# Performance work log

Hardware: AMD Instinct MI355X
Metric: run time of the kernel (lower is better)

Reference implementation:

```python
import jax, jax.numpy as jnp
import numpy as np


def _unfold(x, kh, kw):
    # torch.nn.functional.unfold ordering: channel-major, then kernel row, then kernel col
    B, C, H, W = x.shape
    Ho, Wo = H - kh + 1, W - kw + 1
    cols = jnp.stack([x[:, :, i:i + Ho, j:j + Wo]
                      for i in range(kh) for j in range(kw)], axis=2)  # [B,C,kh*kw,Ho,Wo]
    return cols.reshape(B, C * kh * kw, Ho * Wo), Ho, Wo


def _conv_unfold_matmul(x, w, b):
    # preprocessing: unfold -> A [B,L,K], B = w.view(O,-1).T [K,O]
    # matmul -> [B,L,O]; postprocessing: transpose, reshape, add bias
    O = w.shape[0]
    kh, kw = w.shape[2], w.shape[3]
    cols, Ho, Wo = _unfold(x, kh, kw)                      # [B,K,L]
    out = jnp.einsum('bkl,ok->bol', cols, w.reshape(O, -1))  # [B,O,L]
    return out.reshape(x.shape[0], O, Ho, Wo) + b[None, :, None, None]


def setup_inputs() -> dict:
    key = jax.random.key(0)
    ks = jax.random.split(key, 9)
    B = 4096
    x = jax.random.normal(ks[0], (B, 1, 28, 28), dtype=jnp.float32)
    w1 = jax.random.normal(ks[1], (10, 1, 10, 10), dtype=jnp.float32) * 0.1
    b1 = jax.random.normal(ks[2], (10,), dtype=jnp.float32) * 0.1
    w2 = jax.random.normal(ks[3], (20, 10, 10, 10), dtype=jnp.float32) * 0.03
    b2 = jax.random.normal(ks[4], (20,), dtype=jnp.float32) * 0.1
    w3 = jax.random.normal(ks[5], (20, 20, 5, 5), dtype=jnp.float32) * 0.04
    b3 = jax.random.normal(ks[6], (20,), dtype=jnp.float32) * 0.1
    wf = jax.random.normal(ks[7], (10, 720), dtype=jnp.float32) * 0.04
    bf = jax.random.normal(ks[8], (10,), dtype=jnp.float32) * 0.1
    return {"x": x, "w1": w1, "b1": b1, "w2": w2, "b2": b2,
            "w3": w3, "b3": b3, "wf": wf, "bf": bf}


def reference(x, w1, b1, w2, b2, w3, b3, wf, bf):
    h = jax.nn.relu(_conv_unfold_matmul(x, w1, b1))   # [B,10,19,19]
    h = jax.nn.relu(_conv_unfold_matmul(h, w2, b2))   # [B,20,10,10]
    h = jax.nn.relu(_conv_unfold_matmul(h, w3, b3))   # [B,20,6,6]
    h = h.reshape(-1, 720)
    return h @ wf.T + bf                               # [B,10]
```

## Files before the change

kernel.cpp:

```cpp
#include <hip/hip_runtime.h>


typedef short s16x4 __attribute__((ext_vector_type(4)));
typedef short s16x8 __attribute__((ext_vector_type(8)));
typedef float f32x4 __attribute__((ext_vector_type(4)));

#define ROW1 248
#define ROW2 248
#define XOFF 4712
#define SM_BYTES 11024

static __device__ __forceinline__ unsigned short f2bf(float f) {
    union { float f; unsigned int u; } v; v.f = f;
    unsigned int u = v.u;
    unsigned int r = (u + 0x7fffu + ((u >> 16) & 1u)) >> 16;
    return (unsigned short)r;
}

static __device__ __forceinline__ s16x8 cat8(s16x4 lo, s16x4 hi) {
    return __builtin_shufflevector(lo, hi, 0, 1, 2, 3, 4, 5, 6, 7);
}

__global__ __launch_bounds__(256) void wprep_k(const float* __restrict__ w1,
                                               const float* __restrict__ w2,
                                               const float* __restrict__ w3,
                                               unsigned short* __restrict__ wbuf) {
    int e = blockIdx.x * 256 + threadIdx.x;
    if (e < 40960) {
        int t = e & 7, lane = (e >> 3) & 63, nt = (e >> 9) & 1;
        int ck = (e >> 10) & 3, i = e >> 12;
        int k = ck * 32 + ((lane >> 4) & 3) * 8 + t;
        int o = nt * 16 + (lane & 15);
        int j = k / 12, c = k % 12;
        float val = (j < 10 && c < 10 && o < 20) ? w2[o * 1000 + c * 100 + i * 10 + j] : 0.f;
        wbuf[e] = f2bf(val);
    } else if (e < 61440) {
        int e2 = e - 40960;
        int t = e2 & 7, lane = (e2 >> 3) & 63, nt = (e2 >> 9) & 1;
        int ck = (e2 >> 10) & 3, i = e2 >> 12;
        int k = ck * 32 + ((lane >> 4) & 3) * 8 + t;
        int o = nt * 16 + (lane & 15);
        int j = k / 20, c = k % 20;
        float val = (j < 5 && o < 20) ? w3[o * 500 + c * 25 + i * 5 + j] : 0.f;
        wbuf[e] = f2bf(val);
    } else {
        int e2 = e - 61440;
        int t = e2 & 7, lane = (e2 >> 3) & 63;
        int kc = (e2 >> 9) % 9, nt = (e2 >> 9) / 9;
        int n = nt * 16 + (lane & 15);
        int k = kc * 32 + ((lane >> 4) & 3) * 8 + t;
        float val = 0.f;
        if (n < 190 && k < 280) {
            int ox = n / 10, o = n - ox * 10;
            int i = k / 28, xc = k - i * 28;
            int j = xc - ox;
            if (j >= 0 && j < 10) val = w1[o * 100 + i * 10 + j];
        }
        wbuf[61440 + e2] = f2bf(val);
    }
}

__global__ __launch_bounds__(128, 4) void fused_k(const float* __restrict__ x,
                                                  const float* __restrict__ b1,
                                                  const unsigned short* __restrict__ wbuf2,
                                                  const unsigned short* __restrict__ wbuf3,
                                                  const unsigned short* __restrict__ wband,
                                                  const float* __restrict__ b2,
                                                  const float* __restrict__ b3,
                                                  const float* __restrict__ wf,
                                                  const float* __restrict__ bf,
                                                  float* __restrict__ out) {
    __shared__ __align__(16) unsigned char smem[SM_BYTES];
    unsigned short* sm16 = (unsigned short*)smem;
    unsigned short* h1  = sm16;
    unsigned short* xbf = sm16 + XOFF;
    unsigned short* h2s = sm16;
    float*          h3s = (float*)smem;
    float*          fcp = (float*)(smem + 2880);

    const int tid = threadIdx.x;
    const int wave = tid >> 6, lane = tid & 63;
    const int b = blockIdx.x;
    const int quad = lane >> 4, lm = lane & 15;

    {
        const float4* src = (const float4*)(x + (size_t)b * 784);
        for (int k = tid; k < 196; k += 128) {
            float4 v = src[k];
            s16x4 p = { (short)f2bf(v.x), (short)f2bf(v.y),
                        (short)f2bf(v.z), (short)f2bf(v.w) };
            *(s16x4*)(xbf + k * 4) = p;
        }
        if (tid < 16) xbf[784 + tid] = 0;
        for (int e = tid; e < 95; e += 128) {
            int row = e / 5, seg = e - row * 5;
            *(s16x4*)(h1 + row * ROW1 + 228 + seg * 4) = (s16x4){0, 0, 0, 0};
        }
        for (int e = tid; e < 361; e += 128) {
            int oy = e / 19, ox = e - oy * 19;
            *(unsigned int*)(h1 + oy * ROW1 + ox * 12 + 10) = 0u;
        }
    }
    __syncthreads();

    {
        int m1 = lm + 16; if (m1 > 18) m1 = 18;
        const unsigned short* ab0 = xbf + lm * 28 + quad * 8;
        const unsigned short* ab1 = xbf + m1 * 28 + quad * 8;
        const unsigned short* wb = wband + lane * 8;
        f32x4 acc1[6][2] = {};
#pragma unroll
        for (int kc = 0; kc < 9; ++kc) {
            s16x8 a0 = cat8(*(const s16x4*)(ab0 + kc * 32),
                            *(const s16x4*)(ab0 + kc * 32 + 4));
            s16x8 a1 = cat8(*(const s16x4*)(ab1 + kc * 32),
                            *(const s16x4*)(ab1 + kc * 32 + 4));
#pragma unroll
            for (int q = 0; q < 6; ++q) {
                int nt = wave * 6 + q;
                s16x8 bw = *(const s16x8*)(wb + (nt * 9 + kc) * 512);
                acc1[q][0] = __builtin_amdgcn_mfma_f32_16x16x32_bf16(a0, bw, acc1[q][0], 0, 0, 0);
                acc1[q][1] = __builtin_amdgcn_mfma_f32_16x16x32_bf16(a1, bw, acc1[q][1], 0, 0, 0);
            }
        }
#pragma unroll
        for (int q = 0; q < 6; ++q) {
            int n = (wave * 6 + q) * 16 + lm;
            if (n < 190) {
                int ox = n / 10, o = n - ox * 10;
                float bias = b1[o];
#pragma unroll
                for (int mt = 0; mt < 2; ++mt) {
#pragma unroll
                    for (int r = 0; r < 4; ++r) {
                        int oy = mt * 16 + quad * 4 + r;
                        if (oy < 19)
                            h1[oy * ROW1 + ox * 12 + o] =
                                f2bf(fmaxf(acc1[q][mt][r] + bias, 0.f));
                    }
                }
            }
        }
    }
    __syncthreads();

    int abase[4];
#pragma unroll
    for (int mt = 0; mt < 4; ++mt) {
        int tg = (wave == 0) ? mt : 4 + mt;
        int m = tg * 16 + lm;
        if (m > 99) m = 99;
        int y = m / 10, xx = m - 10 * y;
        abase[mt] = y * ROW1 + xx * 12 + quad * 8;
    }
    f32x4 acc[4][2] = {};
    {
        const unsigned short* wptr = wbuf2 + lane * 8;
        s16x8 wc0 = *(const s16x8*)(wptr);
        s16x8 wc1 = *(const s16x8*)(wptr + 512);
        s16x8 afc[4], afn[4];
        {
            const unsigned short* sbi = h1;
#pragma unroll
            for (int mt = 0; mt < 3; ++mt)
                afc[mt] = cat8(*(const s16x4*)(sbi + abase[mt]),
                               *(const s16x4*)(sbi + abase[mt] + 4));
            if (wave == 0)
                afc[3] = cat8(*(const s16x4*)(sbi + abase[3]),
                              *(const s16x4*)(sbi + abase[3] + 4));
            else
                afc[3] = afc[2];
        }
#pragma unroll
        for (int it = 0; it < 40; ++it) {
            s16x8 wn0 = *(const s16x8*)(wptr + (it + 1) * 1024);
            s16x8 wn1 = *(const s16x8*)(wptr + (it + 1) * 1024 + 512);
            const unsigned short* sbn = h1 + ((it + 1) >> 2) * ROW1 + ((it + 1) & 3) * 32;
#pragma unroll
            for (int mt = 0; mt < 3; ++mt)
                afn[mt] = cat8(*(const s16x4*)(sbn + abase[mt]),
                               *(const s16x4*)(sbn + abase[mt] + 4));
            if (wave == 0)
                afn[3] = cat8(*(const s16x4*)(sbn + abase[3]),
                              *(const s16x4*)(sbn + abase[3] + 4));
            else
                afn[3] = afc[3];
#pragma unroll
            for (int mt = 0; mt < 3; ++mt) {
                acc[mt][0] = __builtin_amdgcn_mfma_f32_16x16x32_bf16(afc[mt], wc0, acc[mt][0], 0, 0, 0);
                acc[mt][1] = __builtin_amdgcn_mfma_f32_16x16x32_bf16(afc[mt], wc1, acc[mt][1], 0, 0, 0);
            }
            if (wave == 0) {
                acc[3][0] = __builtin_amdgcn_mfma_f32_16x16x32_bf16(afc[3], wc0, acc[3][0], 0, 0, 0);
                acc[3][1] = __builtin_amdgcn_mfma_f32_16x16x32_bf16(afc[3], wc1, acc[3][1], 0, 0, 0);
            }
            wc0 = wn0; wc1 = wn1;
#pragma unroll
            for (int mt = 0; mt < 4; ++mt) afc[mt] = afn[mt];
        }
    }
    __syncthreads();

    for (int e = tid; e < 120; e += 128) {
        int row = e / 12, seg = e - row * 12;
        *(s16x4*)(h2s + row * ROW2 + 200 + seg * 4) = (s16x4){0, 0, 0, 0};
    }
#pragma unroll
    for (int mt = 0; mt < 4; ++mt) {
        int tg = (wave == 0) ? mt : 4 + mt;
        if (wave == 0 || mt < 3) {
#pragma unroll
            for (int nt = 0; nt < 2; ++nt) {
                int o = nt * 16 + lm;
                if (o < 20) {
                    float bias = b2[o];
#pragma unroll
                    for (int r = 0; r < 4; ++r) {
                        int pos = tg * 16 + quad * 4 + r;
                        if (pos < 100) {
                            int y2 = pos / 10, x2 = pos - 10 * y2;
                            h2s[y2 * ROW2 + x2 * 20 + o] =
                                f2bf(fmaxf(acc[mt][nt][r] + bias, 0.f));
                        }
                    }
                }
            }
        }
    }
    __syncthreads();

    int abase3[2];
    {
        int tg0 = (wave == 0) ? 0 : 2;
        int m0 = tg0 * 16 + lm; if (m0 > 35) m0 = 35;
        int oy0 = m0 / 6, ox0 = m0 - 6 * oy0;
        abase3[0] = oy0 * ROW2 + ox0 * 20 + quad * 8;
        int m1 = 16 + lm; if (m1 > 35) m1 = 35;
        int oy1 = m1 / 6, ox1 = m1 - 6 * oy1;
        abase3[1] = oy1 * ROW2 + ox1 * 20 + quad * 8;
    }
    f32x4 acc3[2][2] = {};
    {
        const unsigned short* wptr = wbuf3 + lane * 8;
        s16x8 wc0 = *(const s16x8*)(wptr);
        s16x8 wc1 = *(const s16x8*)(wptr + 512);
        s16x8 afc[2], afn[2];
        {
            const unsigned short* sbi = h2s;
            afc[0] = cat8(*(const s16x4*)(sbi + abase3[0]),
                          *(const s16x4*)(sbi + abase3[0] + 4));
            if (wave == 0)
                afc[1] = cat8(*(const s16x4*)(sbi + abase3[1]),
                              *(const s16x4*)(sbi + abase3[1] + 4));
            else
                afc[1] = afc[0];
        }
#pragma unroll
        for (int it = 0; it < 20; ++it) {
            s16x8 wn0 = *(const s16x8*)(wptr + (it + 1) * 1024);
            s16x8 wn1 = *(const s16x8*)(wptr + (it + 1) * 1024 + 512);
            const unsigned short* sbn = h2s + ((it + 1) >> 2) * ROW2 + ((it + 1) & 3) * 32;
            afn[0] = cat8(*(const s16x4*)(sbn + abase3[0]),
                          *(const s16x4*)(sbn + abase3[0] + 4));
            if (wave == 0)
                afn[1] = cat8(*(const s16x4*)(sbn + abase3[1]),
                              *(const s16x4*)(sbn + abase3[1] + 4));
            else
                afn[1] = afc[1];
            acc3[0][0] = __builtin_amdgcn_mfma_f32_16x16x32_bf16(afc[0], wc0, acc3[0][0], 0, 0, 0);
            acc3[0][1] = __builtin_amdgcn_mfma_f32_16x16x32_bf16(afc[0], wc1, acc3[0][1], 0, 0, 0);
            if (wave == 0) {
                acc3[1][0] = __builtin_amdgcn_mfma_f32_16x16x32_bf16(afc[1], wc0, acc3[1][0], 0, 0, 0);
                acc3[1][1] = __builtin_amdgcn_mfma_f32_16x16x32_bf16(afc[1], wc1, acc3[1][1], 0, 0, 0);
            }
            wc0 = wn0; wc1 = wn1;
            afc[0] = afn[0]; afc[1] = afn[1];
        }
    }
    __syncthreads();

#pragma unroll
    for (int mt = 0; mt < 2; ++mt) {
        int tg = (mt == 0) ? ((wave == 0) ? 0 : 2) : 1;
        if (wave == 0 || mt < 1) {
#pragma unroll
            for (int nt = 0; nt < 2; ++nt) {
                int o = nt * 16 + lm;
                if (o < 20) {
                    float b3v = b3[o];
#pragma unroll
                    for (int r = 0; r < 4; ++r) {
                        int pos = tg * 16 + quad * 4 + r;
                        if (pos < 36)
                            h3s[o * 36 + pos] = fmaxf(acc3[mt][nt][r] + b3v, 0.f);
                    }
                }
            }
        }
    }
    __syncthreads();

    float part[10];
#pragma unroll
    for (int n = 0; n < 10; ++n) part[n] = 0.f;
#pragma unroll 1
    for (int s = 0; s < 6; ++s) {
        int k = s * 128 + tid;
        if (k < 720) {
            float v = h3s[k];
#pragma unroll
            for (int n = 0; n < 10; ++n)
                part[n] = fmaf(v, wf[n * 720 + k], part[n]);
        }
    }
#pragma unroll
    for (int n = 0; n < 10; ++n) {
#pragma unroll
        for (int off = 32; off >= 1; off >>= 1)
            part[n] += __shfl_xor(part[n], off, 64);
    }
    if (lane == 0) {
#pragma unroll
        for (int n = 0; n < 10; ++n) fcp[wave * 10 + n] = part[n];
    }
    __syncthreads();
    if (tid < 10)
        out[(size_t)b * 10 + tid] = fcp[tid] + fcp[10 + tid] + bf[tid];
}

extern "C" void kernel_launch(void* const* d_in, const int* in_sizes, int n_in,
                              void* d_out, int out_size, void* d_ws, size_t ws_size,
                              hipStream_t stream) {
    (void)n_in; (void)out_size; (void)ws_size;
    const float* x  = (const float*)d_in[0];
    const float* w1 = (const float*)d_in[1];
    const float* b1 = (const float*)d_in[2];
    const float* w2 = (const float*)d_in[3];
    const float* b2 = (const float*)d_in[4];
    const float* w3 = (const float*)d_in[5];
    const float* b3 = (const float*)d_in[6];
    const float* wf = (const float*)d_in[7];
    const float* bf = (const float*)d_in[8];
    float* out = (float*)d_out;

    const int B = in_sizes[0] / 784;

    unsigned short* wbuf = (unsigned short*)d_ws;

    wprep_k<<<456, 256, 0, stream>>>(w1, w2, w3, wbuf);
    fused_k<<<B, 128, 0, stream>>>(x, b1, wbuf, wbuf + 40960, wbuf + 61440,
                                   b2, b3, wf, bf, out);
}
```

Before: 146.5 us.

## Process two images per block with one wave per image in later layers

Each block now handles two images. Layer 1 is computed jointly for both images, sharing weight loads across four M-tiles. Layers 2 and 3 and the FC head are then split so each wave owns one image end to end, which removes the inter-wave barriers and the uneven tile split. The block count is halved and shared memory roughly doubles, which may reduce occupancy and raises register pressure from the 7x2 accumulator array. The odd-B tail is not handled.

```diff
diff --git a/kernel.cpp b/kernel.cpp
--- a/kernel.cpp
+++ b/kernel.cpp
@@ -7,8 +7,10 @@
 
 #define ROW1 248
 #define ROW2 248
-#define XOFF 4712
-#define SM_BYTES 11024
+#define H1SZ 4712
+#define H2SZ 2480
+#define XOFF 9424
+#define SM_BYTES 22048
 
 static __device__ __forceinline__ unsigned short f2bf(float f) {
     union { float f; unsigned int u; } v; v.f = f;
@@ -74,69 +76,82 @@
     unsigned short* sm16 = (unsigned short*)smem;
     unsigned short* h1  = sm16;
     unsigned short* xbf = sm16 + XOFF;
-    unsigned short* h2s = sm16;
-    float*          h3s = (float*)smem;
-    float*          fcp = (float*)(smem + 2880);
 
     const int tid = threadIdx.x;
     const int wave = tid >> 6, lane = tid & 63;
-    const int b = blockIdx.x;
+    const int b0 = blockIdx.x * 2;
     const int quad = lane >> 4, lm = lane & 15;
 
     {
-        const float4* src = (const float4*)(x + (size_t)b * 784);
-        for (int k = tid; k < 196; k += 128) {
+        const float4* src = (const float4*)(x + (size_t)b0 * 784);
+        for (int k = tid; k < 392; k += 128) {
             float4 v = src[k];
+            int img = (k >= 196);
+            int idx = k - img * 196;
             s16x4 p = { (short)f2bf(v.x), (short)f2bf(v.y),
                         (short)f2bf(v.z), (short)f2bf(v.w) };
-            *(s16x4*)(xbf + k * 4) = p;
-        }
-        if (tid < 16) xbf[784 + tid] = 0;
-        for (int e = tid; e < 95; e += 128) {
-            int row = e / 5, seg = e - row * 5;
-            *(s16x4*)(h1 + row * ROW1 + 228 + seg * 4) = (s16x4){0, 0, 0, 0};
-        }
-        for (int e = tid; e < 361; e += 128) {
-            int oy = e / 19, ox = e - oy * 19;
-            *(unsigned int*)(h1 + oy * ROW1 + ox * 12 + 10) = 0u;
+            *(s16x4*)(xbf + img * 800 + idx * 4) = p;
+        }
+        if (tid < 32) xbf[(tid >> 4) * 800 + 784 + (tid & 15)] = 0;
+        for (int e = tid; e < 190; e += 128) {
+            int img = (e >= 95); int e2 = e - img * 95;
+            int row = e2 / 5, seg = e2 - row * 5;
+            *(s16x4*)(h1 + img * H1SZ + row * ROW1 + 228 + seg * 4) = (s16x4){0, 0, 0, 0};
+        }
+        for (int e = tid; e < 722; e += 128) {
+            int img = (e >= 361); int e2 = e - img * 361;
+            int oy = e2 / 19, ox = e2 - oy * 19;
+            *(unsigned int*)(h1 + img * H1SZ + oy * ROW1 + ox * 12 + 10) = 0u;
         }
     }
     __syncthreads();
 
     {
-        int m1 = lm + 16; if (m1 > 18) m1 = 18;
-        const unsigned short* ab0 = xbf + lm * 28 + quad * 8;
-        const unsigned short* ab1 = xbf + m1 * 28 + quad * 8;
+        int ab[4];
+        {
+            int r0 = lm;
+            int r1 = lm + 16; if (r1 > 18) r1 = 18;
+            ab[0] = r0 * 28 + quad * 8;
+            ab[1] = r1 * 28 + quad * 8;
+            ab[2] = 800 + r0 * 28 + quad * 8;
+            ab[3] = 800 + r1 * 28 + quad * 8;
+        }
         const unsigned short* wb = wband + lane * 8;
-        f32x4 acc1[6][2] = {};
-#pragma unroll
-        for (int kc = 0; kc < 9; ++kc) {
-            s16x8 a0 = cat8(*(const s16x4*)(ab0 + kc * 32),
-                            *(const s16x4*)(ab0 + kc * 32 + 4));
-            s16x8 a1 = cat8(*(const s16x4*)(ab1 + kc * 32),
-                            *(const s16x4*)(ab1 + kc * 32 + 4));
-#pragma unroll
-            for (int q = 0; q < 6; ++q) {
-                int nt = wave * 6 + q;
-                s16x8 bw = *(const s16x8*)(wb + (nt * 9 + kc) * 512);
-                acc1[q][0] = __builtin_amdgcn_mfma_f32_16x16x32_bf16(a0, bw, acc1[q][0], 0, 0, 0);
-                acc1[q][1] = __builtin_amdgcn_mfma_f32_16x16x32_bf16(a1, bw, acc1[q][1], 0, 0, 0);
-            }
-        }
-#pragma unroll
-        for (int q = 0; q < 6; ++q) {
-            int n = (wave * 6 + q) * 16 + lm;
-            if (n < 190) {
-                int ox = n / 10, o = n - ox * 10;
-                float bias = b1[o];
-#pragma unroll
-                for (int mt = 0; mt < 2; ++mt) {
-#pragma unroll
-                    for (int r = 0; r < 4; ++r) {
-                        int oy = mt * 16 + quad * 4 + r;
-                        if (oy < 19)
-                            h1[oy * ROW1 + ox * 12 + o] =
-                                f2bf(fmaxf(acc1[q][mt][r] + bias, 0.f));
+#pragma unroll
+        for (int g = 0; g < 2; ++g) {
+            f32x4 acc1[3][4] = {};
+#pragma unroll
+            for (int kc = 0; kc < 9; ++kc) {
+                s16x8 a[4];
+#pragma unroll
+                for (int mt = 0; mt < 4; ++mt)
+                    a[mt] = cat8(*(const s16x4*)(xbf + ab[mt] + kc * 32),
+                                 *(const s16x4*)(xbf + ab[mt] + kc * 32 + 4));
+#pragma unroll
+                for (int q = 0; q < 3; ++q) {
+                    int nt = wave * 6 + g * 3 + q;
+                    s16x8 bw = *(const s16x8*)(wb + (nt * 9 + kc) * 512);
+#pragma unroll
+                    for (int mt = 0; mt < 4; ++mt)
+                        acc1[q][mt] = __builtin_amdgcn_mfma_f32_16x16x32_bf16(a[mt], bw, acc1[q][mt], 0, 0, 0);
+                }
+            }
+#pragma unroll
+            for (int q = 0; q < 3; ++q) {
+                int n = (wave * 6 + g * 3 + q) * 16 + lm;
+                if (n < 190) {
+                    int ox = n / 10, o = n - ox * 10;
+                    float bias = b1[o];
+#pragma unroll
+                    for (int mt = 0; mt < 4; ++mt) {
+                        int img = mt >> 1, half = mt & 1;
+#pragma unroll
+                        for (int r = 0; r < 4; ++r) {
+                            int oy = half * 16 + quad * 4 + r;
+                            if (oy < 19)
+                                h1[img * H1SZ + oy * ROW1 + ox * 12 + o] =
+                                    f2bf(fmaxf(acc1[q][mt][r] + bias, 0.f));
+                        }
                     }
                 }
             }
@@ -144,170 +159,121 @@
     }
     __syncthreads();
 
-    int abase[4];
-#pragma unroll
-    for (int mt = 0; mt < 4; ++mt) {
-        int tg = (wave == 0) ? mt : 4 + mt;
-        int m = tg * 16 + lm;
-        if (m > 99) m = 99;
+    const unsigned short* h1w = h1 + wave * H1SZ;
+    int abase[7];
+#pragma unroll
+    for (int mt = 0; mt < 7; ++mt) {
+        int m = mt * 16 + lm; if (m > 99) m = 99;
         int y = m / 10, xx = m - 10 * y;
         abase[mt] = y * ROW1 + xx * 12 + quad * 8;
     }
-    f32x4 acc[4][2] = {};
+    f32x4 acc[7][2] = {};
     {
         const unsigned short* wptr = wbuf2 + lane * 8;
         s16x8 wc0 = *(const s16x8*)(wptr);
         s16x8 wc1 = *(const s16x8*)(wptr + 512);
-        s16x8 afc[4], afn[4];
-        {
-            const unsigned short* sbi = h1;
-#pragma unroll
-            for (int mt = 0; mt < 3; ++mt)
-                afc[mt] = cat8(*(const s16x4*)(sbi + abase[mt]),
-                               *(const s16x4*)(sbi + abase[mt] + 4));
-            if (wave == 0)
-                afc[3] = cat8(*(const s16x4*)(sbi + abase[3]),
-                              *(const s16x4*)(sbi + abase[3] + 4));
-            else
-                afc[3] = afc[2];
-        }
 #pragma unroll
         for (int it = 0; it < 40; ++it) {
             s16x8 wn0 = *(const s16x8*)(wptr + (it + 1) * 1024);
             s16x8 wn1 = *(const s16x8*)(wptr + (it + 1) * 1024 + 512);
-            const unsigned short* sbn = h1 + ((it + 1) >> 2) * ROW1 + ((it + 1) & 3) * 32;
-#pragma unroll
-            for (int mt = 0; mt < 3; ++mt)
-                afn[mt] = cat8(*(const s16x4*)(sbn + abase[mt]),
-                               *(const s16x4*)(sbn + abase[mt] + 4));
-            if (wave == 0)
-                afn[3] = cat8(*(const s16x4*)(sbn + abase[3]),
-                              *(const s16x4*)(sbn + abase[3] + 4));
-            else
-                afn[3] = afc[3];
-#pragma unroll
-            for (int mt = 0; mt < 3; ++mt) {
-                acc[mt][0] = __builtin_amdgcn_mfma_f32_16x16x32_bf16(afc[mt], wc0, acc[mt][0], 0, 0, 0);
-                acc[mt][1] = __builtin_amdgcn_mfma_f32_16x16x32_bf16(afc[mt], wc1, acc[mt][1], 0, 0, 0);
-            }
-            if (wave == 0) {
-                acc[3][0] = __builtin_amdgcn_mfma_f32_16x16x32_bf16(afc[3], wc0, acc[3][0], 0, 0, 0);
-                acc[3][1] = __builtin_amdgcn_mfma_f32_16x16x32_bf16(afc[3], wc1, acc[3][1], 0, 0, 0);
+            const unsigned short* sb = h1w + (it >> 2) * ROW1 + (it & 3) * 32;
+            s16x8 af[7];
+#pragma unroll
+            for (int mt = 0; mt < 7; ++mt)
+                af[mt] = cat8(*(const s16x4*)(sb + abase[mt]),
+                              *(const s16x4*)(sb + abase[mt] + 4));
+#pragma unroll
+            for (int mt = 0; mt < 7; ++mt) {
+                acc[mt][0] = __builtin_amdgcn_mfma_f32_16x16x32_bf16(af[mt], wc0, acc[mt][0], 0, 0, 0);
+                acc[mt][1] = __builtin_amdgcn_mfma_f32_16x16x32_bf16(af[mt], wc1, acc[mt][1], 0, 0, 0);
             }
             wc0 = wn0; wc1 = wn1;
-#pragma unroll
-            for (int mt = 0; mt < 4; ++mt) afc[mt] = afn[mt];
         }
     }
     __syncthreads();
 
-    for (int e = tid; e < 120; e += 128) {
+    unsigned short* h2w = sm16 + wave * H2SZ;
+    for (int e = lane; e < 120; e += 64) {
         int row = e / 12, seg = e - row * 12;
-        *(s16x4*)(h2s + row * ROW2 + 200 + seg * 4) = (s16x4){0, 0, 0, 0};
-    }
-#pragma unroll
-    for (int mt = 0; mt < 4; ++mt) {
-        int tg = (wave == 0) ? mt : 4 + mt;
-        if (wave == 0 || mt < 3) {
-#pragma unroll
-            for (int nt = 0; nt < 2; ++nt) {
-                int o = nt * 16 + lm;
-                if (o < 20) {
-                    float bias = b2[o];
-#pragma unroll
-                    for (int r = 0; r < 4; ++r) {
-                        int pos = tg * 16 + quad * 4 + r;
-                        if (pos < 100) {
-                            int y2 = pos / 10, x2 = pos - 10 * y2;
-                            h2s[y2 * ROW2 + x2 * 20 + o] =
-                                f2bf(fmaxf(acc[mt][nt][r] + bias, 0.f));
-                        }
+        *(s16x4*)(h2w + row * ROW2 + 200 + seg * 4) = (s16x4){0, 0, 0, 0};
+    }
+#pragma unroll
+    for (int mt = 0; mt < 7; ++mt) {
+#pragma unroll
+        for (int nt = 0; nt < 2; ++nt) {
+            int o = nt * 16 + lm;
+            if (o < 20) {
+                float bias = b2[o];
+#pragma unroll
+                for (int r = 0; r < 4; ++r) {
+                    int pos = mt * 16 + quad * 4 + r;
+                    if (pos < 100) {
+                        int y2 = pos / 10, x2 = pos - 10 * y2;
+                        h2w[y2 * ROW2 + x2 * 20 + o] =
+                            f2bf(fmaxf(acc[mt][nt][r] + bias, 0.f));
                     }
                 }
             }
         }
     }
-    __syncthreads();
-
-    int abase3[2];
-    {
-        int tg0 = (wave == 0) ? 0 : 2;
-        int m0 = tg0 * 16 + lm; if (m0 > 35) m0 = 35;
-        int oy0 = m0 / 6, ox0 = m0 - 6 * oy0;
-        abase3[0] = oy0 * ROW2 + ox0 * 20 + quad * 8;
-        int m1 = 16 + lm; if (m1 > 35) m1 = 35;
-        int oy1 = m1 / 6, ox1 = m1 - 6 * oy1;
-        abase3[1] = oy1 * ROW2 + ox1 * 20 + quad * 8;
-    }
-    f32x4 acc3[2][2] = {};
+
+    int abase3[3];
+#pragma unroll
+    for (int mt = 0; mt < 3; ++mt) {
+        int m = mt * 16 + lm; if (m > 35) m = 35;
+        int oy = m / 6, ox = m - 6 * oy;
+        abase3[mt] = oy * ROW2 + ox * 20 + quad * 8;
+    }
+    f32x4 acc3[3][2] = {};
     {
         const unsigned short* wptr = wbuf3 + lane * 8;
         s16x8 wc0 = *(const s16x8*)(wptr);
         s16x8 wc1 = *(const s16x8*)(wptr + 512);
-        s16x8 afc[2], afn[2];
-        {
-            const unsigned short* sbi = h2s;
-            afc[0] = cat8(*(const s16x4*)(sbi + abase3[0]),
-                          *(const s16x4*)(sbi + abase3[0] + 4));
-            if (wave == 0)
-                afc[1] = cat8(*(const s16x4*)(sbi + abase3[1]),
-                              *(const s16x4*)(sbi + abase3[1] + 4));
-            else
-                afc[1] = afc[0];
-        }
 #pragma unroll
         for (int it = 0; it < 20; ++it) {
             s16x8 wn0 = *(const s16x8*)(wptr + (it + 1) * 1024);
             s16x8 wn1 = *(const s16x8*)(wptr + (it + 1) * 1024 + 512);
-            const unsigned short* sbn = h2s + ((it + 1) >> 2) * ROW2 + ((it + 1) & 3) * 32;
-            afn[0] = cat8(*(const s16x4*)(sbn + abase3[0]),
-                          *(const s16x4*)(sbn + abase3[0] + 4));
-            if (wave == 0)
-                afn[1] = cat8(*(const s16x4*)(sbn + abase3[1]),
-                              *(const s16x4*)(sbn + abase3[1] + 4));
-            else
-                afn[1] = afc[1];
-            acc3[0][0] = __builtin_amdgcn_mfma_f32_16x16x32_bf16(afc[0], wc0, acc3[0][0], 0, 0, 0);
-            acc3[0][1] = __builtin_amdgcn_mfma_f32_16x16x32_bf16(afc[0], wc1, acc3[0][1], 0, 0, 0);
-            if (wave == 0) {
-                acc3[1][0] = __builtin_amdgcn_mfma_f32_16x16x32_bf16(afc[1], wc0, acc3[1][0], 0, 0, 0);
-                acc3[1][1] = __builtin_amdgcn_mfma_f32_16x16x32_bf16(afc[1], wc1, acc3[1][1], 0, 0, 0);
+            const unsigned short* sb = h2w + (it >> 2) * ROW2 + (it & 3) * 32;
+            s16x8 af[3];
+#pragma unroll
+            for (int mt = 0; mt < 3; ++mt)
+                af[mt] = cat8(*(const s16x4*)(sb + abase3[mt]),
+                              *(const s16x4*)(sb + abase3[mt] + 4));
+#pragma unroll
+            for (int mt = 0; mt < 3; ++mt) {
+                acc3[mt][0] = __builtin_amdgcn_mfma_f32_16x16x32_bf16(af[mt], wc0, acc3[mt][0], 0, 0, 0);
+                acc3[mt][1] = __builtin_amdgcn_mfma_f32_16x16x32_bf16(af[mt], wc1, acc3[mt][1], 0, 0, 0);
             }
             wc0 = wn0; wc1 = wn1;
-            afc[0] = afn[0]; afc[1] = afn[1];
-        }
-    }
-    __syncthreads();
-
-#pragma unroll
-    for (int mt = 0; mt < 2; ++mt) {
-        int tg = (mt == 0) ? ((wave == 0) ? 0 : 2) : 1;
-        if (wave == 0 || mt < 1) {
-#pragma unroll
-            for (int nt = 0; nt < 2; ++nt) {
-                int o = nt * 16 + lm;
-                if (o < 20) {
-                    float b3v = b3[o];
-#pragma unroll
-                    for (int r = 0; r < 4; ++r) {
-                        int pos = tg * 16 + quad * 4 + r;
-                        if (pos < 36)
-                            h3s[o * 36 + pos] = fmaxf(acc3[mt][nt][r] + b3v, 0.f);
-                    }
+        }
+    }
+
+    float* h3w = (float*)(smem + wave * (H2SZ * 2));
+#pragma unroll
+    for (int mt = 0; mt < 3; ++mt) {
+#pragma unroll
+        for (int nt = 0; nt < 2; ++nt) {
+            int o = nt * 16 + lm;
+            if (o < 20) {
+                float b3v = b3[o];
+#pragma unroll
+                for (int r = 0; r < 4; ++r) {
+                    int pos = mt * 16 + quad * 4 + r;
+                    if (pos < 36)
+                        h3w[o * 36 + pos] = fmaxf(acc3[mt][nt][r] + b3v, 0.f);
                 }
             }
         }
     }
-    __syncthreads();
 
     float part[10];
 #pragma unroll
     for (int n = 0; n < 10; ++n) part[n] = 0.f;
 #pragma unroll 1
-    for (int s = 0; s < 6; ++s) {
-        int k = s * 128 + tid;
+    for (int s = 0; s < 12; ++s) {
+        int k = s * 64 + lane;
         if (k < 720) {
-            float v = h3s[k];
+            float v = h3w[k];
 #pragma unroll
             for (int n = 0; n < 10; ++n)
                 part[n] = fmaf(v, wf[n * 720 + k], part[n]);
@@ -320,12 +286,10 @@
             part[n] += __shfl_xor(part[n], off, 64);
     }
     if (lane == 0) {
-#pragma unroll
-        for (int n = 0; n < 10; ++n) fcp[wave * 10 + n] = part[n];
-    }
-    __syncthreads();
-    if (tid < 10)
-        out[(size_t)b * 10 + tid] = fcp[tid] + fcp[10 + tid] + bf[tid];
+        float* dst = out + (size_t)(b0 + wave) * 10;
+#pragma unroll
+        for (int n = 0; n < 10; ++n) dst[n] = part[n] + bf[n];
+    }
 }
 
 extern "C" void kernel_launch(void* const* d_in, const int* in_sizes, int n_in,
@@ -348,6 +312,6 @@
     unsigned short* wbuf = (unsigned short*)d_ws;
 
     wprep_k<<<456, 256, 0, stream>>>(w1, w2, w3, wbuf);
-    fused_k<<<B, 128, 0, stream>>>(x, b1, wbuf, wbuf + 40960, wbuf + 61440,
-                                   b2, b3, wf, bf, out);
-}
+    fused_k<<<B / 2, 128, 0, stream>>>(x, b1, wbuf, wbuf + 40960, wbuf + 61440,
+                                       b2, b3, wf, bf, out);
+}
```

Measured after the change: 147.1 us. About the same (+0.5%).
